# Performance work log

Measured on AMD Instinct MI355X. Metric: run time of the kernel, lower is better.

The kernel has to match this reference:

```python
import jax, jax.numpy as jnp
import numpy as np

INPUT_DIM, HIDDEN_DIM, OUTPUT_DIM, NUM_LAYERS = 128, 512, 128, 2
B, T = 32, 2048


def setup_inputs() -> dict:
    key = jax.random.key(0)
    ks = jax.random.split(key, 11)
    s_in = 1.0 / np.sqrt(HIDDEN_DIM)
    inp = {"x": jax.random.normal(ks[0], (B, T, INPUT_DIM), dtype=jnp.float32)}
    # layer 0 (input_dim -> hidden), layer 1 (hidden -> hidden); PyTorch gate order i,f,g,o
    inp["w_ih0"] = jax.random.uniform(ks[1], (4 * HIDDEN_DIM, INPUT_DIM), minval=-s_in, maxval=s_in)
    inp["w_hh0"] = jax.random.uniform(ks[2], (4 * HIDDEN_DIM, HIDDEN_DIM), minval=-s_in, maxval=s_in)
    inp["b_ih0"] = jax.random.uniform(ks[3], (4 * HIDDEN_DIM,), minval=-s_in, maxval=s_in)
    inp["b_hh0"] = jax.random.uniform(ks[4], (4 * HIDDEN_DIM,), minval=-s_in, maxval=s_in)
    inp["w_ih1"] = jax.random.uniform(ks[5], (4 * HIDDEN_DIM, HIDDEN_DIM), minval=-s_in, maxval=s_in)
    inp["w_hh1"] = jax.random.uniform(ks[6], (4 * HIDDEN_DIM, HIDDEN_DIM), minval=-s_in, maxval=s_in)
    inp["b_ih1"] = jax.random.uniform(ks[7], (4 * HIDDEN_DIM,), minval=-s_in, maxval=s_in)
    inp["b_hh1"] = jax.random.uniform(ks[8], (4 * HIDDEN_DIM,), minval=-s_in, maxval=s_in)
    inp["fc_w"] = jax.random.uniform(ks[9], (OUTPUT_DIM, HIDDEN_DIM), minval=-s_in, maxval=s_in)
    inp["fc_b"] = jax.random.uniform(ks[10], (OUTPUT_DIM,), minval=-s_in, maxval=s_in)
    return inp


def _lstm_layer(x, w_ih, w_hh, b_ih, b_hh):
    # x: [B, T, D] -> hidden states [B, T, H], final (h, c) each [B, H]
    b, t, _ = x.shape
    h4 = w_hh.shape[0]
    H = h4 // 4
    # precompute input projections for all timesteps (one big GEMM)
    x_proj = jnp.einsum('btd,gd->btg', x, w_ih) + b_ih + b_hh  # [B, T, 4H]

    def step(carry, xt):
        h, c = carry
        gates = xt + h @ w_hh.T  # [B, 4H]
        i, f, g, o = jnp.split(gates, 4, axis=-1)
        i = jax.nn.sigmoid(i)
        f = jax.nn.sigmoid(f)
        g = jnp.tanh(g)
        o = jax.nn.sigmoid(o)
        c = f * c + i * g
        h = o * jnp.tanh(c)
        return (h, c), h

    init = (jnp.zeros((b, H), x.dtype), jnp.zeros((b, H), x.dtype))
    (h_n, c_n), hs = jax.lax.scan(step, init, jnp.swapaxes(x_proj, 0, 1))
    return jnp.swapaxes(hs, 0, 1), h_n, c_n


def reference(x, w_ih0, w_hh0, b_ih0, b_hh0, w_ih1, w_hh1, b_ih1, b_hh1, fc_w, fc_b):
    out0, h0, c0 = _lstm_layer(x, w_ih0, w_hh0, b_ih0, b_hh0)
    out1, h1, c1 = _lstm_layer(out0, w_ih1, w_hh1, b_ih1, b_hh1)
    h_n = jnp.stack([h0, h1])  # [L, B, H]
    c_n = jnp.stack([c0, c1])  # [L, B, H]
    # fc(relu(.)) applied once over all (batch, time) -- collapses the Python loop
    output = jnp.einsum('bth,oh->bto', jax.nn.relu(out1), fc_w) + fc_b  # [B, T, O]
    hidden = jnp.einsum('lbh,oh->lbo', jax.nn.relu(h_n), fc_w) + fc_b   # [L, B, O]
    return jnp.squeeze(output), hidden, c_n
```

## Files before the change

kernel.cpp:

```cpp
#include <hip/hip_runtime.h>

typedef unsigned int u32;
typedef unsigned short u16;
typedef unsigned long long u64;

#define T_STEPS 2048
#define BATCH   32
#define HID     512
#define INDIM   128
#define OUTD    128
#define NG      2048
#define L0_WGS  64
#define L1_WGS  64
#define FC_WGS  4
#define NWG     (L0_WGS + L1_WGS + FC_WGS)
#define BH      (BATCH * HID)

#define HID_OFF 8388608
#define CN_OFF  8396800

#define WS_FLAGS   0
#define WS_H0RING  16384
#define WS_H1RING  (WS_H0RING + 131072)
#define WS_BIAS0   (WS_H1RING + 131072)
#define WS_BIAS1   (WS_BIAS0 + 8192)
#define WS_WFC     (WS_BIAS1 + 8192)
#define WS_WL0     (WS_WFC + 131072)
#define WS_WL1     (WS_WL0 + 2621440)
#define WS_XBF     (WS_WL1 + 4194304)

typedef __bf16 bf16x8 __attribute__((ext_vector_type(8)));
typedef float  f32x4  __attribute__((ext_vector_type(4)));
typedef unsigned int u32x4 __attribute__((ext_vector_type(4)));

__device__ __forceinline__ u16 f2bf(float f) {
    u32 u = __float_as_uint(f);
    u32 r = u + 0x7FFFu + ((u >> 16) & 1u);
    return (u16)(r >> 16);
}

union UB2 { u32x4 u; bf16x8 b; };
__device__ __forceinline__ bf16x8 as_bf(u32x4 u) { UB2 x; x.u = u; return x.b; }

__device__ __forceinline__ u32 relu2(u32 u) {
    u32 lo = (u & 0x8000u)     ? 0u : (u & 0xFFFFu);
    u32 hi = (u & 0x80000000u) ? 0u : (u & 0xFFFF0000u);
    return lo | hi;
}

__device__ __forceinline__ u32x4 ld16_llc(const void* p) {
    u32x4 r;
    asm volatile("global_load_dwordx4 %0, %1, off sc0 sc1"
                 : "=v"(r) : "v"(p) : "memory");
    return r;
}
__device__ __forceinline__ void wait_vm0() {
    asm volatile("s_waitcnt vmcnt(0)" ::: "memory");
    __builtin_amdgcn_sched_barrier(0);
}
__device__ __forceinline__ void vm0() {
    asm volatile("s_waitcnt vmcnt(0)" ::: "memory");
}


__global__ void k_zero(u32* dst, int n) {
    int i = blockIdx.x * blockDim.x + threadIdx.x;
    if (i < n) dst[i] = 0u;
}

__global__ void k_bias(const float* __restrict__ bih0, const float* __restrict__ bhh0,
                       const float* __restrict__ bih1, const float* __restrict__ bhh1,
                       float* __restrict__ bias0, float* __restrict__ bias1) {
    int i = blockIdx.x * blockDim.x + threadIdx.x;
    if (i < NG) {
        int orig = (i & 3) * HID + (i >> 2);
        bias0[i] = bih0[orig] + bhh0[orig];
        bias1[i] = bih1[orig] + bhh1[orig];
    }
}

__global__ void k_xconv(const float* __restrict__ x, u16* __restrict__ xbf) {
    int i = blockIdx.x * blockDim.x + threadIdx.x;
    float4 v = reinterpret_cast<const float4*>(x)[i];
    u32 lo = (u32)f2bf(v.x) | ((u32)f2bf(v.y) << 16);
    u32 hi = (u32)f2bf(v.z) | ((u32)f2bf(v.w) << 16);
    reinterpret_cast<uint2*>(xbf)[i] = make_uint2(lo, hi);
}

__global__ void k_wconv(const float* __restrict__ wih0, const float* __restrict__ whh0,
                        const float* __restrict__ wih1, const float* __restrict__ whh1,
                        const float* __restrict__ fcw,
                        u16* __restrict__ wl0, u16* __restrict__ wl1, u16* __restrict__ wfc) {
    int i = blockIdx.x * blockDim.x + threadIdx.x;
    if (i < 64 * 20480) {
        int wg = i / 20480, r = i % 20480;
        int ks = r / 1024, kb = (r % 1024) / 256, n = (r % 256) / 8, j = r % 8;
        int k = ks * 32 + kb * 8 + j;
        int p = wg * 32 + n;
        int orig = (p & 3) * HID + (p >> 2);
        float v = (k < HID) ? whh0[orig * HID + k] : wih0[orig * INDIM + (k - HID)];
        wl0[i] = f2bf(v);
        return;
    }
    int i1 = i - 64 * 20480;
    if (i1 < 64 * 32768) {
        int wg = i1 / 32768, r = i1 % 32768;
        int ks = r / 1024, kb = (r % 1024) / 256, n = (r % 256) / 8, j = r % 8;
        int k = ks * 32 + kb * 8 + j;
        int p = wg * 32 + n;
        int orig = (p & 3) * HID + (p >> 2);
        float v = (k < HID) ? wih1[orig * HID + k] : whh1[orig * HID + (k - HID)];
        wl1[i1] = f2bf(v);
        return;
    }
    int i2 = i1 - 64 * 32768;
    if (i2 < 4 * 16384) {
        int wg = i2 / 16384, r = i2 % 16384;
        int ks = r / 1024, kb = (r % 1024) / 256, n = (r % 256) / 8, j = r % 8;
        int k = ks * 32 + kb * 8 + j;
        int o = wg * 32 + n;
        wfc[i2] = f2bf(fcw[o * HID + k]);
    }
}


__global__ __launch_bounds__(256, 1)
void k_lstm(const u16* __restrict__ xbf,
            const u16* __restrict__ wl0g, const u16* __restrict__ wl1g, const u16* __restrict__ wfcg,
            const float* __restrict__ bias0, const float* __restrict__ bias1, const float* __restrict__ fcb,
            u16* __restrict__ h0ring, u16* __restrict__ h1ring,
            u32* __restrict__ flags, float* __restrict__ dout)
{
    __shared__ u16   wlds[32768];
    __shared__ u32x4 hstage[2][2048];
    const int tid  = threadIdx.x;
    const int lane = tid & 63;
    const int wv   = tid >> 6;
    const int mt   = wv >> 1;
    const int nt   = wv & 1;
    const int ci   = lane & 15;
    const int quad = lane >> 4;
    const int wg   = blockIdx.x;

    int role, rwg;
    if      (wg < L0_WGS)           { role = 0; rwg = wg; }
    else if (wg < L0_WGS + L1_WGS)  { role = 1; rwg = wg - L0_WGS; }
    else                            { role = 2; rwg = wg - L0_WGS - L1_WGS; }

    u32* flagL0 = flags;
    u32* flagL1 = flags + 64 * 16;
    u32* flagFC = flags + 128 * 16;
    u32* myflag = flags + wg * 16;

    {
        const u16* src = (role == 0) ? (wl0g + rwg * 20480)
                       : (role == 1) ? (wl1g + rwg * 32768)
                                     : (wfcg + rwg * 16384);
        const int n4 = (role == 0) ? 2560 : (role == 1) ? 4096 : 2048;
        uint4* d4 = reinterpret_cast<uint4*>(wlds);
        const uint4* s4 = reinterpret_cast<const uint4*>(src);
        for (int i = tid; i < n4; i += 256) d4[i] = s4[i];
    }
    __syncthreads();

    const bf16x8* wp = reinterpret_cast<const bf16x8*>(wlds);
    const int wbase  = quad * 32 + nt * 16 + ci;
    const int pcol   = rwg * 32 + nt * 16 + ci;
    const int gateid = pcol & 3;
    const float bias = (role == 0) ? bias0[pcol] : (role == 1) ? bias1[pcol] : fcb[pcol];
    const int brow0  = mt * 16 + quad * 4;
    const int arow   = mt * 16 + ci;
    const int jidx   = pcol >> 2;
    const int hfrag  = arow * 64 + quad;
    const int hswz   = arow & 7;

    float cst[4] = {0.f, 0.f, 0.f, 0.f};

    auto spin = [&](u32* f, int target) {
        if (target > 0)
            while ((int)__hip_atomic_load(f, __ATOMIC_RELAXED, __HIP_MEMORY_SCOPE_AGENT) < target)
                __builtin_amdgcn_s_sleep(1);
    };

    auto stage1 = [&](const u16* slot, int buf) {
        u32x4 b[8];
        #pragma unroll
        for (int r = 0; r < 8; ++r) b[r] = ld16_llc(slot + (tid + r * 256) * 8);
        wait_vm0();
        #pragma unroll
        for (int r = 0; r < 8; ++r) {
            int c = tid + r * 256;
            hstage[buf][c ^ ((c >> 6) & 7)] = b[r];
        }
    };
    auto stage2 = [&](const u16* s0, const u16* s1) {
        u32x4 b0[8], b1[8];
        #pragma unroll
        for (int r = 0; r < 8; ++r) b0[r] = ld16_llc(s0 + (tid + r * 256) * 8);
        #pragma unroll
        for (int r = 0; r < 8; ++r) b1[r] = ld16_llc(s1 + (tid + r * 256) * 8);
        wait_vm0();
        #pragma unroll
        for (int r = 0; r < 8; ++r) {
            int c = tid + r * 256;
            int cs = c ^ ((c >> 6) & 7);
            hstage[0][cs] = b0[r];
            hstage[1][cs] = b1[r];
        }
    };

    auto epi = [&](const f32x4& acc, u16* slotb) {
        float ga[4], hv[4];
        #pragma unroll
        for (int r = 0; r < 4; ++r) {
            float g  = acc[r] + bias;
            float sv = 1.0f / (1.0f + __expf(-g));
            float tv = 1.0f - 2.0f / (__expf(2.0f * g) + 1.0f);
            ga[r] = (gateid == 2) ? tv : sv;
        }
        const int bl = lane & ~3;
        #pragma unroll
        for (int r = 0; r < 4; ++r) {
            float iv = __shfl(ga[r], bl + 0);
            float fv = __shfl(ga[r], bl + 1);
            float gv = __shfl(ga[r], bl + 2);
            float ov = __shfl(ga[r], bl + 3);
            float cn = fv * cst[r] + iv * gv;
            cst[r] = cn;
            hv[r] = ov * (1.0f - 2.0f / (__expf(2.0f * cn) + 1.0f));
        }
        u32 lo = 0, hi = 0;
        #pragma unroll
        for (int r = 0; r < 4; ++r) {
            float c0 = __shfl(hv[r], (quad << 4) + 0);
            float c1 = __shfl(hv[r], (quad << 4) + 4);
            float c2 = __shfl(hv[r], (quad << 4) + 8);
            float c3 = __shfl(hv[r], (quad << 4) + 12);
            if (ci == r) {
                lo = (u32)f2bf(c0) | ((u32)f2bf(c1) << 16);
                hi = (u32)f2bf(c2) | ((u32)f2bf(c3) << 16);
            }
        }
        if (ci < 4) {
            u64* dst = reinterpret_cast<u64*>(slotb) + (brow0 + ci) * 128 + rwg * 2 + nt;
            u64 val = (u64)lo | ((u64)hi << 32);
            __hip_atomic_store(dst, val, __ATOMIC_RELAXED, __HIP_MEMORY_SCOPE_AGENT);
        }
    };

    #define HMFMA16S(BUF, KSOFF)                                                 \
        _Pragma("unroll")                                                        \
        for (int _k = 0; _k < 16; ++_k) {                                        \
          u32x4 _hv = hstage[BUF][(hfrag + _k * 4) ^ hswz];                      \
          bf16x8 _bv = wp[wbase + (_k + (KSOFF)) * 128];                         \
          if (_k & 1) accB = __builtin_amdgcn_mfma_f32_16x16x32_bf16(as_bf(_hv), _bv, accB, 0, 0, 0); \
          else        accA = __builtin_amdgcn_mfma_f32_16x16x32_bf16(as_bf(_hv), _bv, accA, 0, 0, 0); \
        }

    auto fcTileS = [&](int buf) -> f32x4 {
        f32x4 accA = {0.f,0.f,0.f,0.f}, accB = {0.f,0.f,0.f,0.f};
        #pragma unroll
        for (int ks = 0; ks < 16; ++ks) {
            u32x4 v = hstage[buf][(hfrag + ks * 4) ^ hswz];
            v[0] = relu2(v[0]); v[1] = relu2(v[1]); v[2] = relu2(v[2]); v[3] = relu2(v[3]);
            bf16x8 bv = wp[wbase + ks * 128];
            if (ks & 1) accB = __builtin_amdgcn_mfma_f32_16x16x32_bf16(as_bf(v), bv, accB, 0, 0, 0);
            else        accA = __builtin_amdgcn_mfma_f32_16x16x32_bf16(as_bf(v), bv, accA, 0, 0, 0);
        }
        return accA + accB;
    };

    if (role == 0) {
        u32* pf = (tid < 64) ? (flagL0 + tid * 16) : (tid < 128) ? (flagL1 + (tid - 64) * 16) : nullptr;
        const int po = (tid < 64) ? 0 : -3;
        for (int t = 0; t < T_STEPS; ++t) {
            const u16* xA = xbf + (arow * T_STEPS + t) * INDIM + quad * 8;
            f32x4 accA = {0.f, 0.f, 0.f, 0.f}, accB = {0.f, 0.f, 0.f, 0.f};
            u32x4 xv[4];
            #pragma unroll
            for (int k4 = 0; k4 < 4; ++k4) xv[k4] = *reinterpret_cast<const u32x4*>(xA + k4 * 32);
            #pragma unroll
            for (int k4 = 0; k4 < 4; ++k4) {
                bf16x8 bv = wp[wbase + (16 + k4) * 128];
                if (k4 & 1) accB = __builtin_amdgcn_mfma_f32_16x16x32_bf16(as_bf(xv[k4]), bv, accB, 0, 0, 0);
                else        accA = __builtin_amdgcn_mfma_f32_16x16x32_bf16(as_bf(xv[k4]), bv, accA, 0, 0, 0);
            }
            if (pf) spin(pf, t + po);
            __syncthreads();
            stage1(h0ring + ((t + 3) & 3) * BH, 0);
            __syncthreads();
            HMFMA16S(0, 0);
            epi(accA + accB, h0ring + (t & 3) * BH);
            vm0();
            __syncthreads();
            if (tid == 0)
                __hip_atomic_store(myflag, (u32)(t + 1), __ATOMIC_RELAXED, __HIP_MEMORY_SCOPE_AGENT);
        }
    } else if (role == 1) {
        u32* pf = (tid < 64)  ? (flagL0 + tid * 16)
                : (tid < 128) ? (flagL1 + (tid - 64) * 16)
                : (tid < 132) ? (flagFC + (tid - 128) * 16) : nullptr;
        const int po = (tid < 64) ? 1 : (tid < 128) ? 0 : -3;
        for (int t = 0; t < T_STEPS; ++t) {
            if (pf) spin(pf, t + po);
            __syncthreads();
            stage2(h0ring + (t & 3) * BH,
                   h1ring + ((t + 3) & 3) * BH);
            __syncthreads();
            f32x4 accA = {0.f, 0.f, 0.f, 0.f}, accB = {0.f, 0.f, 0.f, 0.f};
            HMFMA16S(0, 0);
            HMFMA16S(1, 16);
            epi(accA + accB, h1ring + (t & 3) * BH);
            vm0();
            __syncthreads();
            if (tid == 0)
                __hip_atomic_store(myflag, (u32)(t + 1), __ATOMIC_RELAXED, __HIP_MEMORY_SCOPE_AGENT);
        }
    } else {
        u32* pf = (tid < 64) ? (flagL1 + tid * 16) : nullptr;
        for (int t = 0; t < T_STEPS; ++t) {
            if (pf) spin(pf, t + 1);
            __syncthreads();
            stage1(h1ring + (t & 3) * BH, 0);
            __syncthreads();
            f32x4 acc = fcTileS(0);
            #pragma unroll
            for (int r = 0; r < 4; ++r)
                dout[((brow0 + r) * T_STEPS + t) * OUTD + pcol] = acc[r] + bias;
            __syncthreads();
            if (tid == 0)
                __hip_atomic_store(myflag, (u32)(t + 1), __ATOMIC_RELAXED, __HIP_MEMORY_SCOPE_AGENT);
        }
        stage1(h0ring + 3 * BH, 1);
        __syncthreads();
        f32x4 hh1 = fcTileS(0);
        f32x4 hh0 = fcTileS(1);
        #pragma unroll
        for (int r = 0; r < 4; ++r)
            dout[HID_OFF + (brow0 + r) * OUTD + pcol] = hh0[r] + bias;
        #pragma unroll
        for (int r = 0; r < 4; ++r)
            dout[HID_OFF + (BATCH + brow0 + r) * OUTD + pcol] = hh1[r] + bias;
    }

    if (role <= 1 && (ci & 3) == 0) {
        #pragma unroll
        for (int r = 0; r < 4; ++r)
            dout[CN_OFF + (role * BATCH + brow0 + r) * HID + jidx] = cst[r];
    }
}


extern "C" void kernel_launch(void* const* d_in, const int* in_sizes, int n_in,
                              void* d_out, int out_size, void* d_ws, size_t ws_size,
                              hipStream_t stream) {
    const float* x    = (const float*)d_in[0];
    const float* wih0 = (const float*)d_in[1];
    const float* whh0 = (const float*)d_in[2];
    const float* bih0 = (const float*)d_in[3];
    const float* bhh0 = (const float*)d_in[4];
    const float* wih1 = (const float*)d_in[5];
    const float* whh1 = (const float*)d_in[6];
    const float* bih1 = (const float*)d_in[7];
    const float* bhh1 = (const float*)d_in[8];
    const float* fcw  = (const float*)d_in[9];
    const float* fcb  = (const float*)d_in[10];

    char* ws = (char*)d_ws;
    u32*  flags = (u32*)(ws + WS_FLAGS);
    u16*  h0r   = (u16*)(ws + WS_H0RING);
    u16*  h1r   = (u16*)(ws + WS_H1RING);
    float* b0   = (float*)(ws + WS_BIAS0);
    float* b1   = (float*)(ws + WS_BIAS1);
    u16*  wfc   = (u16*)(ws + WS_WFC);
    u16*  wl0   = (u16*)(ws + WS_WL0);
    u16*  wl1   = (u16*)(ws + WS_WL1);
    u16*  xbf   = (u16*)(ws + WS_XBF);
    float* dout = (float*)d_out;

    k_zero<<<272, 256, 0, stream>>>((u32*)ws, 69632);
    k_bias<<<8, 256, 0, stream>>>(bih0, bhh0, bih1, bhh1, b0, b1);
    k_xconv<<<8192, 256, 0, stream>>>(x, xbf);
    k_wconv<<<13568, 256, 0, stream>>>(wih0, whh0, wih1, whh1, fcw, wl0, wl1, wfc);
    k_lstm<<<NWG, 256, 0, stream>>>(xbf, wl0, wl1, wfc, b0, b1, fcb,
                                    h0r, h1r, flags, dout);
}
```

Measured before the change: 8.986 ms.

## Use full-length hidden-state history buffers to drop ring backpressure waits

When the workspace is large enough, each layer writes its hidden states to a distinct slot per timestep instead of a 4-deep ring. This removes the backpressure spins where producers waited on consumers (layer 0 on layer 1, layer 1 on the FC workgroups), so the three pipeline stages can drift apart freely. Because no slot is ever rewritten, loads switch from LLC-coherent sc0 sc1 to sc0 only. The cost is about 128 MB of extra workspace, and the new path only runs if the harness supplies that much.

After: 9.059 ms. About the same (+0.8%).

```diff
diff --git a/kernel.cpp b/kernel.cpp
--- a/kernel.cpp
+++ b/kernel.cpp
@@ -28,6 +28,9 @@
 #define WS_WL0     (WS_WFC + 131072)
 #define WS_WL1     (WS_WL0 + 2621440)
 #define WS_XBF     (WS_WL1 + 4194304)
+#define WS_H0DEEP  (WS_XBF + 16777216)
+#define WS_H1DEEP  (WS_H0DEEP + 67141632)
+#define WS_DEEPEND (WS_H1DEEP + 67141632)
 
 typedef __bf16 bf16x8 __attribute__((ext_vector_type(8)));
 typedef float  f32x4  __attribute__((ext_vector_type(4)));
@@ -51,6 +54,12 @@
 __device__ __forceinline__ u32x4 ld16_llc(const void* p) {
     u32x4 r;
     asm volatile("global_load_dwordx4 %0, %1, off sc0 sc1"
+                 : "=v"(r) : "v"(p) : "memory");
+    return r;
+}
+__device__ __forceinline__ u32x4 ld16_l2(const void* p) {
+    u32x4 r;
+    asm volatile("global_load_dwordx4 %0, %1, off sc0"
                  : "=v"(r) : "v"(p) : "memory");
     return r;
 }
@@ -129,7 +138,7 @@
             const u16* __restrict__ wl0g, const u16* __restrict__ wl1g, const u16* __restrict__ wfcg,
             const float* __restrict__ bias0, const float* __restrict__ bias1, const float* __restrict__ fcb,
             u16* __restrict__ h0ring, u16* __restrict__ h1ring,
-            u32* __restrict__ flags, float* __restrict__ dout)
+            u32* __restrict__ flags, float* __restrict__ dout, const int deep)
 {
     __shared__ u16   wlds[32768];
     __shared__ u32x4 hstage[2][2048];
@@ -182,10 +191,19 @@
                 __builtin_amdgcn_s_sleep(1);
     };
 
+    auto rdIdx = [&](int t_h) -> long {
+        return deep ? (long)(t_h + 1) : (long)(t_h & 3);
+    };
+
     auto stage1 = [&](const u16* slot, int buf) {
         u32x4 b[8];
-        #pragma unroll
-        for (int r = 0; r < 8; ++r) b[r] = ld16_llc(slot + (tid + r * 256) * 8);
+        if (deep) {
+            #pragma unroll
+            for (int r = 0; r < 8; ++r) b[r] = ld16_l2(slot + (tid + r * 256) * 8);
+        } else {
+            #pragma unroll
+            for (int r = 0; r < 8; ++r) b[r] = ld16_llc(slot + (tid + r * 256) * 8);
+        }
         wait_vm0();
         #pragma unroll
         for (int r = 0; r < 8; ++r) {
@@ -195,10 +213,17 @@
     };
     auto stage2 = [&](const u16* s0, const u16* s1) {
         u32x4 b0[8], b1[8];
-        #pragma unroll
-        for (int r = 0; r < 8; ++r) b0[r] = ld16_llc(s0 + (tid + r * 256) * 8);
-        #pragma unroll
-        for (int r = 0; r < 8; ++r) b1[r] = ld16_llc(s1 + (tid + r * 256) * 8);
+        if (deep) {
+            #pragma unroll
+            for (int r = 0; r < 8; ++r) b0[r] = ld16_l2(s0 + (tid + r * 256) * 8);
+            #pragma unroll
+            for (int r = 0; r < 8; ++r) b1[r] = ld16_l2(s1 + (tid + r * 256) * 8);
+        } else {
+            #pragma unroll
+            for (int r = 0; r < 8; ++r) b0[r] = ld16_llc(s0 + (tid + r * 256) * 8);
+            #pragma unroll
+            for (int r = 0; r < 8; ++r) b1[r] = ld16_llc(s1 + (tid + r * 256) * 8);
+        }
         wait_vm0();
         #pragma unroll
         for (int r = 0; r < 8; ++r) {
@@ -271,7 +296,8 @@
     };
 
     if (role == 0) {
-        u32* pf = (tid < 64) ? (flagL0 + tid * 16) : (tid < 128) ? (flagL1 + (tid - 64) * 16) : nullptr;
+        u32* pf = (tid < 64) ? (flagL0 + tid * 16)
+                : (!deep && tid < 128) ? (flagL1 + (tid - 64) * 16) : nullptr;
         const int po = (tid < 64) ? 0 : -3;
         for (int t = 0; t < T_STEPS; ++t) {
             const u16* xA = xbf + (arow * T_STEPS + t) * INDIM + quad * 8;
@@ -287,10 +313,10 @@
             }
             if (pf) spin(pf, t + po);
             __syncthreads();
-            stage1(h0ring + ((t + 3) & 3) * BH, 0);
+            stage1(h0ring + rdIdx(t - 1) * BH, 0);
             __syncthreads();
             HMFMA16S(0, 0);
-            epi(accA + accB, h0ring + (t & 3) * BH);
+            epi(accA + accB, h0ring + rdIdx(t) * BH);
             vm0();
             __syncthreads();
             if (tid == 0)
@@ -299,18 +325,18 @@
     } else if (role == 1) {
         u32* pf = (tid < 64)  ? (flagL0 + tid * 16)
                 : (tid < 128) ? (flagL1 + (tid - 64) * 16)
-                : (tid < 132) ? (flagFC + (tid - 128) * 16) : nullptr;
+                : (!deep && tid < 132) ? (flagFC + (tid - 128) * 16) : nullptr;
         const int po = (tid < 64) ? 1 : (tid < 128) ? 0 : -3;
         for (int t = 0; t < T_STEPS; ++t) {
             if (pf) spin(pf, t + po);
             __syncthreads();
-            stage2(h0ring + (t & 3) * BH,
-                   h1ring + ((t + 3) & 3) * BH);
+            stage2(h0ring + rdIdx(t) * BH,
+                   h1ring + rdIdx(t - 1) * BH);
             __syncthreads();
             f32x4 accA = {0.f, 0.f, 0.f, 0.f}, accB = {0.f, 0.f, 0.f, 0.f};
             HMFMA16S(0, 0);
             HMFMA16S(1, 16);
-            epi(accA + accB, h1ring + (t & 3) * BH);
+            epi(accA + accB, h1ring + rdIdx(t) * BH);
             vm0();
             __syncthreads();
             if (tid == 0)
@@ -321,7 +347,7 @@
         for (int t = 0; t < T_STEPS; ++t) {
             if (pf) spin(pf, t + 1);
             __syncthreads();
-            stage1(h1ring + (t & 3) * BH, 0);
+            stage1(h1ring + rdIdx(t) * BH, 0);
             __syncthreads();
             f32x4 acc = fcTileS(0);
             #pragma unroll
@@ -331,7 +357,7 @@
             if (tid == 0)
                 __hip_atomic_store(myflag, (u32)(t + 1), __ATOMIC_RELAXED, __HIP_MEMORY_SCOPE_AGENT);
         }
-        stage1(h0ring + 3 * BH, 1);
+        stage1(h0ring + rdIdx(T_STEPS - 1) * BH, 1);
         __syncthreads();
         f32x4 hh1 = fcTileS(0);
         f32x4 hh0 = fcTileS(1);
@@ -368,8 +394,6 @@
 
     char* ws = (char*)d_ws;
     u32*  flags = (u32*)(ws + WS_FLAGS);
-    u16*  h0r   = (u16*)(ws + WS_H0RING);
-    u16*  h1r   = (u16*)(ws + WS_H1RING);
     float* b0   = (float*)(ws + WS_BIAS0);
     float* b1   = (float*)(ws + WS_BIAS1);
     u16*  wfc   = (u16*)(ws + WS_WFC);
@@ -378,10 +402,20 @@
     u16*  xbf   = (u16*)(ws + WS_XBF);
     float* dout = (float*)d_out;
 
-    k_zero<<<272, 256, 0, stream>>>((u32*)ws, 69632);
+    const int deep = (ws_size >= (size_t)WS_DEEPEND) ? 1 : 0;
+    u16* h0r = deep ? (u16*)(ws + WS_H0DEEP) : (u16*)(ws + WS_H0RING);
+    u16* h1r = deep ? (u16*)(ws + WS_H1DEEP) : (u16*)(ws + WS_H1RING);
+
+    if (deep) {
+        k_zero<<<16, 256, 0, stream>>>((u32*)ws, 4096);
+        k_zero<<<32, 256, 0, stream>>>((u32*)(ws + WS_H0DEEP), 8192);
+        k_zero<<<32, 256, 0, stream>>>((u32*)(ws + WS_H1DEEP), 8192);
+    } else {
+        k_zero<<<272, 256, 0, stream>>>((u32*)ws, 69632);
+    }
     k_bias<<<8, 256, 0, stream>>>(bih0, bhh0, bih1, bhh1, b0, b1);
     k_xconv<<<8192, 256, 0, stream>>>(x, xbf);
     k_wconv<<<13568, 256, 0, stream>>>(wih0, whh0, wih1, whh1, fcw, wl0, wl1, wfc);
     k_lstm<<<NWG, 256, 0, stream>>>(xbf, wl0, wl1, wfc, b0, b1, fcb,
-                                    h0r, h1r, flags, dout);
-}
+                                    h0r, h1r, flags, dout, deep);
+}
```

## Halve persistent workgroup count with 512-thread blocks and stream layer-1 weights

Applied to the files above, without the earlier changes.

Restructures the persistent LSTM kernel to use half as many workgroups (32+32+2) with 512 threads each, so every block owns 64 gate columns. Fewer participants in each step's flag barrier should shorten the per-step cross-workgroup sync. Layer 1 now keeps only half its weights in LDS and reads the recurrent half from global memory. It also splits its staging so the MFMAs on the first h buffer run while the second load is still in flight. Layer 0 moves the input-projection MFMAs for the next step off the critical path, after the epilogue. The cost is more work per block per step and extra global weight traffic for layer 1.

New measurement: 10.58 ms. +17.7%, slower.

```diff
diff --git a/kernel.cpp b/kernel.cpp
--- a/kernel.cpp
+++ b/kernel.cpp
@@ -10,10 +10,11 @@
 #define INDIM   128
 #define OUTD    128
 #define NG      2048
-#define L0_WGS  64
-#define L1_WGS  64
-#define FC_WGS  4
+#define L0_WGS  32
+#define L1_WGS  32
+#define FC_WGS  2
 #define NWG     (L0_WGS + L1_WGS + FC_WGS)
+#define NTHR    512
 #define BH      (BATCH * HID)
 
 #define HID_OFF 8388608
@@ -58,6 +59,10 @@
     asm volatile("s_waitcnt vmcnt(0)" ::: "memory");
     __builtin_amdgcn_sched_barrier(0);
 }
+__device__ __forceinline__ void wait_vm4() {
+    asm volatile("s_waitcnt vmcnt(4)" ::: "memory");
+    __builtin_amdgcn_sched_barrier(0);
+}
 __device__ __forceinline__ void vm0() {
     asm volatile("s_waitcnt vmcnt(0)" ::: "memory");
 }
@@ -92,52 +97,52 @@
                         const float* __restrict__ fcw,
                         u16* __restrict__ wl0, u16* __restrict__ wl1, u16* __restrict__ wfc) {
     int i = blockIdx.x * blockDim.x + threadIdx.x;
-    if (i < 64 * 20480) {
-        int wg = i / 20480, r = i % 20480;
-        int ks = r / 1024, kb = (r % 1024) / 256, n = (r % 256) / 8, j = r % 8;
+    if (i < 32 * 40960) {
+        int wg = i / 40960, r = i % 40960;
+        int ks = r / 2048, kb = (r % 2048) / 512, n = (r % 512) / 8, j = r % 8;
         int k = ks * 32 + kb * 8 + j;
-        int p = wg * 32 + n;
+        int p = wg * 64 + n;
         int orig = (p & 3) * HID + (p >> 2);
         float v = (k < HID) ? whh0[orig * HID + k] : wih0[orig * INDIM + (k - HID)];
         wl0[i] = f2bf(v);
         return;
     }
-    int i1 = i - 64 * 20480;
-    if (i1 < 64 * 32768) {
-        int wg = i1 / 32768, r = i1 % 32768;
-        int ks = r / 1024, kb = (r % 1024) / 256, n = (r % 256) / 8, j = r % 8;
+    int i1 = i - 32 * 40960;
+    if (i1 < 32 * 65536) {
+        int wg = i1 / 65536, r = i1 % 65536;
+        int ks = r / 2048, kb = (r % 2048) / 512, n = (r % 512) / 8, j = r % 8;
         int k = ks * 32 + kb * 8 + j;
-        int p = wg * 32 + n;
+        int p = wg * 64 + n;
         int orig = (p & 3) * HID + (p >> 2);
         float v = (k < HID) ? wih1[orig * HID + k] : whh1[orig * HID + (k - HID)];
         wl1[i1] = f2bf(v);
         return;
     }
-    int i2 = i1 - 64 * 32768;
-    if (i2 < 4 * 16384) {
-        int wg = i2 / 16384, r = i2 % 16384;
-        int ks = r / 1024, kb = (r % 1024) / 256, n = (r % 256) / 8, j = r % 8;
+    int i2 = i1 - 32 * 65536;
+    if (i2 < 2 * 32768) {
+        int wg = i2 / 32768, r = i2 % 32768;
+        int ks = r / 2048, kb = (r % 2048) / 512, n = (r % 512) / 8, j = r % 8;
         int k = ks * 32 + kb * 8 + j;
-        int o = wg * 32 + n;
+        int o = wg * 64 + n;
         wfc[i2] = f2bf(fcw[o * HID + k]);
     }
 }
 
 
-__global__ __launch_bounds__(256, 1)
+__global__ __launch_bounds__(NTHR, 1)
 void k_lstm(const u16* __restrict__ xbf,
             const u16* __restrict__ wl0g, const u16* __restrict__ wl1g, const u16* __restrict__ wfcg,
             const float* __restrict__ bias0, const float* __restrict__ bias1, const float* __restrict__ fcb,
             u16* __restrict__ h0ring, u16* __restrict__ h1ring,
             u32* __restrict__ flags, float* __restrict__ dout)
 {
-    __shared__ u16   wlds[32768];
-    __shared__ u32x4 hstage[2][2048];
+    __shared__ u16   wlds[40960];
+    __shared__ u32x4 hstage[2048];
     const int tid  = threadIdx.x;
     const int lane = tid & 63;
     const int wv   = tid >> 6;
-    const int mt   = wv >> 1;
-    const int nt   = wv & 1;
+    const int mt   = wv >> 2;
+    const int nc   = wv & 3;
     const int ci   = lane & 15;
     const int quad = lane >> 4;
     const int wg   = blockIdx.x;
@@ -150,22 +155,23 @@
     u32* flagL0 = flags;
     u32* flagL1 = flags + 64 * 16;
     u32* flagFC = flags + 128 * 16;
-    u32* myflag = flags + wg * 16;
+    u32* myflag = (role == 0) ? (flagL0 + rwg * 16)
+                : (role == 1) ? (flagL1 + rwg * 16) : (flagFC + rwg * 16);
 
     {
-        const u16* src = (role == 0) ? (wl0g + rwg * 20480)
-                       : (role == 1) ? (wl1g + rwg * 32768)
-                                     : (wfcg + rwg * 16384);
-        const int n4 = (role == 0) ? 2560 : (role == 1) ? 4096 : 2048;
+        const u16* src = (role == 0) ? (wl0g + rwg * 40960)
+                       : (role == 1) ? (wl1g + rwg * 65536)
+                                     : (wfcg + rwg * 32768);
+        const int n4 = (role == 0) ? 5120 : 4096;
         uint4* d4 = reinterpret_cast<uint4*>(wlds);
         const uint4* s4 = reinterpret_cast<const uint4*>(src);
-        for (int i = tid; i < n4; i += 256) d4[i] = s4[i];
+        for (int i = tid; i < n4; i += NTHR) d4[i] = s4[i];
     }
     __syncthreads();
 
     const bf16x8* wp = reinterpret_cast<const bf16x8*>(wlds);
-    const int wbase  = quad * 32 + nt * 16 + ci;
-    const int pcol   = rwg * 32 + nt * 16 + ci;
+    const int wbase  = quad * 64 + nc * 16 + ci;
+    const int pcol   = rwg * 64 + nc * 16 + ci;
     const int gateid = pcol & 3;
     const float bias = (role == 0) ? bias0[pcol] : (role == 1) ? bias1[pcol] : fcb[pcol];
     const int brow0  = mt * 16 + quad * 4;
@@ -181,32 +187,19 @@
             while ((int)__hip_atomic_load(f, __ATOMIC_RELAXED, __HIP_MEMORY_SCOPE_AGENT) < target)
                 __builtin_amdgcn_s_sleep(1);
     };
-
-    auto stage1 = [&](const u16* slot, int buf) {
-        u32x4 b[8];
-        #pragma unroll
-        for (int r = 0; r < 8; ++r) b[r] = ld16_llc(slot + (tid + r * 256) * 8);
+    auto stf = [&](u32* f, u32 v) {
+        __hip_atomic_store(f, v, __ATOMIC_RELAXED, __HIP_MEMORY_SCOPE_AGENT);
+    };
+
+    auto scat = [&](int c, u32x4 b) { hstage[c ^ ((c >> 6) & 7)] = b; };
+
+    auto stage1 = [&](const u16* slot) {
+        u32x4 b[4];
+        #pragma unroll
+        for (int r = 0; r < 4; ++r) b[r] = ld16_llc(slot + (tid + r * 512) * 8);
         wait_vm0();
         #pragma unroll
-        for (int r = 0; r < 8; ++r) {
-            int c = tid + r * 256;
-            hstage[buf][c ^ ((c >> 6) & 7)] = b[r];
-        }
-    };
-    auto stage2 = [&](const u16* s0, const u16* s1) {
-        u32x4 b0[8], b1[8];
-        #pragma unroll
-        for (int r = 0; r < 8; ++r) b0[r] = ld16_llc(s0 + (tid + r * 256) * 8);
-        #pragma unroll
-        for (int r = 0; r < 8; ++r) b1[r] = ld16_llc(s1 + (tid + r * 256) * 8);
-        wait_vm0();
-        #pragma unroll
-        for (int r = 0; r < 8; ++r) {
-            int c = tid + r * 256;
-            int cs = c ^ ((c >> 6) & 7);
-            hstage[0][cs] = b0[r];
-            hstage[1][cs] = b1[r];
-        }
+        for (int r = 0; r < 4; ++r) scat(tid + r * 512, b[r]);
     };
 
     auto epi = [&](const f32x4& acc, u16* slotb) {
@@ -242,28 +235,28 @@
             }
         }
         if (ci < 4) {
-            u64* dst = reinterpret_cast<u64*>(slotb) + (brow0 + ci) * 128 + rwg * 2 + nt;
+            u64* dst = reinterpret_cast<u64*>(slotb) + (brow0 + ci) * 128 + rwg * 4 + nc;
             u64 val = (u64)lo | ((u64)hi << 32);
             __hip_atomic_store(dst, val, __ATOMIC_RELAXED, __HIP_MEMORY_SCOPE_AGENT);
         }
     };
 
-    #define HMFMA16S(BUF, KSOFF)                                                 \
+    #define HMFMA16L(KSOFF)                                                      \
         _Pragma("unroll")                                                        \
         for (int _k = 0; _k < 16; ++_k) {                                        \
-          u32x4 _hv = hstage[BUF][(hfrag + _k * 4) ^ hswz];                      \
-          bf16x8 _bv = wp[wbase + (_k + (KSOFF)) * 128];                         \
+          u32x4 _hv = hstage[(hfrag + _k * 4) ^ hswz];                           \
+          bf16x8 _bv = wp[wbase + (_k + (KSOFF)) * 256];                         \
           if (_k & 1) accB = __builtin_amdgcn_mfma_f32_16x16x32_bf16(as_bf(_hv), _bv, accB, 0, 0, 0); \
           else        accA = __builtin_amdgcn_mfma_f32_16x16x32_bf16(as_bf(_hv), _bv, accA, 0, 0, 0); \
         }
 
-    auto fcTileS = [&](int buf) -> f32x4 {
+    auto fcTileS = [&]() -> f32x4 {
         f32x4 accA = {0.f,0.f,0.f,0.f}, accB = {0.f,0.f,0.f,0.f};
         #pragma unroll
         for (int ks = 0; ks < 16; ++ks) {
-            u32x4 v = hstage[buf][(hfrag + ks * 4) ^ hswz];
+            u32x4 v = hstage[(hfrag + ks * 4) ^ hswz];
             v[0] = relu2(v[0]); v[1] = relu2(v[1]); v[2] = relu2(v[2]); v[3] = relu2(v[3]);
-            bf16x8 bv = wp[wbase + ks * 128];
+            bf16x8 bv = wp[wbase + ks * 256];
             if (ks & 1) accB = __builtin_amdgcn_mfma_f32_16x16x32_bf16(as_bf(v), bv, accB, 0, 0, 0);
             else        accA = __builtin_amdgcn_mfma_f32_16x16x32_bf16(as_bf(v), bv, accA, 0, 0, 0);
         }
@@ -271,70 +264,97 @@
     };
 
     if (role == 0) {
-        u32* pf = (tid < 64) ? (flagL0 + tid * 16) : (tid < 128) ? (flagL1 + (tid - 64) * 16) : nullptr;
-        const int po = (tid < 64) ? 0 : -3;
-        for (int t = 0; t < T_STEPS; ++t) {
+        u32* pf = (tid < 32) ? (flagL0 + tid * 16)
+                : (tid >= 64 && tid < 96) ? (flagL1 + (tid - 64) * 16) : nullptr;
+        const int po = (tid < 32) ? 0 : -3;
+        auto xpart = [&](int t, f32x4& aA, f32x4& aB) {
             const u16* xA = xbf + (arow * T_STEPS + t) * INDIM + quad * 8;
-            f32x4 accA = {0.f, 0.f, 0.f, 0.f}, accB = {0.f, 0.f, 0.f, 0.f};
             u32x4 xv[4];
             #pragma unroll
             for (int k4 = 0; k4 < 4; ++k4) xv[k4] = *reinterpret_cast<const u32x4*>(xA + k4 * 32);
             #pragma unroll
             for (int k4 = 0; k4 < 4; ++k4) {
-                bf16x8 bv = wp[wbase + (16 + k4) * 128];
-                if (k4 & 1) accB = __builtin_amdgcn_mfma_f32_16x16x32_bf16(as_bf(xv[k4]), bv, accB, 0, 0, 0);
-                else        accA = __builtin_amdgcn_mfma_f32_16x16x32_bf16(as_bf(xv[k4]), bv, accA, 0, 0, 0);
+                bf16x8 bv = wp[wbase + (16 + k4) * 256];
+                if (k4 & 1) aB = __builtin_amdgcn_mfma_f32_16x16x32_bf16(as_bf(xv[k4]), bv, aB, 0, 0, 0);
+                else        aA = __builtin_amdgcn_mfma_f32_16x16x32_bf16(as_bf(xv[k4]), bv, aA, 0, 0, 0);
             }
-            if (pf) spin(pf, t + po);
-            __syncthreads();
-            stage1(h0ring + ((t + 3) & 3) * BH, 0);
-            __syncthreads();
-            HMFMA16S(0, 0);
-            epi(accA + accB, h0ring + (t & 3) * BH);
-            vm0();
-            __syncthreads();
-            if (tid == 0)
-                __hip_atomic_store(myflag, (u32)(t + 1), __ATOMIC_RELAXED, __HIP_MEMORY_SCOPE_AGENT);
-        }
-    } else if (role == 1) {
-        u32* pf = (tid < 64)  ? (flagL0 + tid * 16)
-                : (tid < 128) ? (flagL1 + (tid - 64) * 16)
-                : (tid < 132) ? (flagFC + (tid - 128) * 16) : nullptr;
-        const int po = (tid < 64) ? 1 : (tid < 128) ? 0 : -3;
+        };
+        f32x4 xA0 = {0.f,0.f,0.f,0.f}, xB0 = {0.f,0.f,0.f,0.f};
+        xpart(0, xA0, xB0);
         for (int t = 0; t < T_STEPS; ++t) {
             if (pf) spin(pf, t + po);
             __syncthreads();
-            stage2(h0ring + (t & 3) * BH,
-                   h1ring + ((t + 3) & 3) * BH);
-            __syncthreads();
-            f32x4 accA = {0.f, 0.f, 0.f, 0.f}, accB = {0.f, 0.f, 0.f, 0.f};
-            HMFMA16S(0, 0);
-            HMFMA16S(1, 16);
+            stage1(h0ring + ((t + 3) & 3) * BH);
+            __syncthreads();
+            f32x4 accA = xA0, accB = xB0;
+            HMFMA16L(0);
+            epi(accA + accB, h0ring + (t & 3) * BH);
+            if (t + 1 < T_STEPS) {
+                xA0 = (f32x4){0.f,0.f,0.f,0.f}; xB0 = (f32x4){0.f,0.f,0.f,0.f};
+                xpart(t + 1, xA0, xB0);
+            }
+            vm0();
+            __syncthreads();
+            if (tid == 0) stf(myflag, (u32)(t + 1));
+        }
+    } else if (role == 1) {
+        u32* pf = (tid < 32)  ? (flagL0 + tid * 16)
+                : (tid >= 64 && tid < 96) ? (flagL1 + (tid - 64) * 16)
+                : (tid >= 128 && tid < 130) ? (flagFC + (tid - 128) * 16) : nullptr;
+        const int po = (tid < 32) ? 1 : (tid < 96) ? 0 : -3;
+        const u16* wB = wl1g + rwg * 65536 + 32768 + quad * 512 + (nc * 16 + ci) * 8;
+        for (int t = 0; t < T_STEPS; ++t) {
+            if (pf) spin(pf, t + po);
+            __syncthreads();
+            const u16* s0 = h0ring + (t & 3) * BH;
+            const u16* s1 = h1ring + ((t + 3) & 3) * BH;
+            u32x4 b0[4], b1[4];
+            #pragma unroll
+            for (int r = 0; r < 4; ++r) b0[r] = ld16_llc(s0 + (tid + r * 512) * 8);
+            #pragma unroll
+            for (int r = 0; r < 4; ++r) b1[r] = ld16_llc(s1 + (tid + r * 512) * 8);
+            wait_vm4();
+            #pragma unroll
+            for (int r = 0; r < 4; ++r) scat(tid + r * 512, b0[r]);
+            __syncthreads();
+            f32x4 accA = {0.f,0.f,0.f,0.f}, accB = {0.f,0.f,0.f,0.f};
+            HMFMA16L(0);
+            __syncthreads();
+            wait_vm0();
+            #pragma unroll
+            for (int r = 0; r < 4; ++r) scat(tid + r * 512, b1[r]);
+            __syncthreads();
+            #pragma unroll
+            for (int _k = 0; _k < 16; ++_k) {
+                u32x4 hv = hstage[(hfrag + _k * 4) ^ hswz];
+                bf16x8 bv = *reinterpret_cast<const bf16x8*>(wB + _k * 2048);
+                if (_k & 1) accB = __builtin_amdgcn_mfma_f32_16x16x32_bf16(as_bf(hv), bv, accB, 0, 0, 0);
+                else        accA = __builtin_amdgcn_mfma_f32_16x16x32_bf16(as_bf(hv), bv, accA, 0, 0, 0);
+            }
             epi(accA + accB, h1ring + (t & 3) * BH);
             vm0();
             __syncthreads();
-            if (tid == 0)
-                __hip_atomic_store(myflag, (u32)(t + 1), __ATOMIC_RELAXED, __HIP_MEMORY_SCOPE_AGENT);
+            if (tid == 0) stf(myflag, (u32)(t + 1));
         }
     } else {
-        u32* pf = (tid < 64) ? (flagL1 + tid * 16) : nullptr;
+        u32* pf = (tid < 32) ? (flagL1 + tid * 16) : nullptr;
         for (int t = 0; t < T_STEPS; ++t) {
             if (pf) spin(pf, t + 1);
             __syncthreads();
-            stage1(h1ring + (t & 3) * BH, 0);
-            __syncthreads();
-            f32x4 acc = fcTileS(0);
+            stage1(h1ring + (t & 3) * BH);
+            __syncthreads();
+            f32x4 acc = fcTileS();
             #pragma unroll
             for (int r = 0; r < 4; ++r)
                 dout[((brow0 + r) * T_STEPS + t) * OUTD + pcol] = acc[r] + bias;
             __syncthreads();
-            if (tid == 0)
-                __hip_atomic_store(myflag, (u32)(t + 1), __ATOMIC_RELAXED, __HIP_MEMORY_SCOPE_AGENT);
-        }
-        stage1(h0ring + 3 * BH, 1);
+            if (tid == 0) stf(myflag, (u32)(t + 1));
+        }
+        f32x4 hh1 = fcTileS();
         __syncthreads();
-        f32x4 hh1 = fcTileS(0);
-        f32x4 hh0 = fcTileS(1);
+        stage1(h0ring + 3 * BH);
+        __syncthreads();
+        f32x4 hh0 = fcTileS();
         #pragma unroll
         for (int r = 0; r < 4; ++r)
             dout[HID_OFF + (brow0 + r) * OUTD + pcol] = hh0[r] + bias;
@@ -382,6 +402,6 @@
     k_bias<<<8, 256, 0, stream>>>(bih0, bhh0, bih1, bhh1, b0, b1);
     k_xconv<<<8192, 256, 0, stream>>>(x, xbf);
     k_wconv<<<13568, 256, 0, stream>>>(wih0, whh0, wih1, whh1, fcw, wl0, wl1, wfc);
-    k_lstm<<<NWG, 256, 0, stream>>>(xbf, wl0, wl1, wfc, b0, b1, fcb,
-                                    h0r, h1r, flags, dout);
-}
+    k_lstm<<<NWG, NTHR, 0, stream>>>(xbf, wl0, wl1, wfc, b0, b1, fcb,
+                                     h0r, h1r, flags, dout);
+}
```

## Per-wave flag spinning, overlap x-projection and ring loads with dependency waits

Applied to the files above, without the earlier changes.

Each wave now polls the producer flags itself (lane-indexed) rather than a subset of threads spinning and then a block barrier, which removes one __syncthreads per step. Layer 0 computes the next step's input projection after the epilogue, taking it off the critical path. Both LSTM roles also issue their global ring loads before waiting on the slack/back-pressure flags. This shortens the serial per-timestep recurrence latency, at the cost of more flag polling traffic and subtler memory-ordering assumptions.

After: 9.252 ms. 3.0% more time.

```diff
diff --git a/kernel.cpp b/kernel.cpp
--- a/kernel.cpp
+++ b/kernel.cpp
@@ -181,32 +181,24 @@
             while ((int)__hip_atomic_load(f, __ATOMIC_RELAXED, __HIP_MEMORY_SCOPE_AGENT) < target)
                 __builtin_amdgcn_s_sleep(1);
     };
-
-    auto stage1 = [&](const u16* slot, int buf) {
-        u32x4 b[8];
-        #pragma unroll
-        for (int r = 0; r < 8; ++r) b[r] = ld16_llc(slot + (tid + r * 256) * 8);
-        wait_vm0();
+    auto stf = [&](u32* f, u32 v) {
+        __hip_atomic_store(f, v, __ATOMIC_RELAXED, __HIP_MEMORY_SCOPE_AGENT);
+    };
+
+    auto scat = [&](int buf, u32x4* b) {
         #pragma unroll
         for (int r = 0; r < 8; ++r) {
             int c = tid + r * 256;
             hstage[buf][c ^ ((c >> 6) & 7)] = b[r];
         }
     };
-    auto stage2 = [&](const u16* s0, const u16* s1) {
-        u32x4 b0[8], b1[8];
-        #pragma unroll
-        for (int r = 0; r < 8; ++r) b0[r] = ld16_llc(s0 + (tid + r * 256) * 8);
-        #pragma unroll
-        for (int r = 0; r < 8; ++r) b1[r] = ld16_llc(s1 + (tid + r * 256) * 8);
+
+    auto stage1 = [&](const u16* slot, int buf) {
+        u32x4 b[8];
+        #pragma unroll
+        for (int r = 0; r < 8; ++r) b[r] = ld16_llc(slot + (tid + r * 256) * 8);
         wait_vm0();
-        #pragma unroll
-        for (int r = 0; r < 8; ++r) {
-            int c = tid + r * 256;
-            int cs = c ^ ((c >> 6) & 7);
-            hstage[0][cs] = b0[r];
-            hstage[1][cs] = b1[r];
-        }
+        scat(buf, b);
     };
 
     auto epi = [&](const f32x4& acc, u16* slotb) {
@@ -271,41 +263,59 @@
     };
 
     if (role == 0) {
-        u32* pf = (tid < 64) ? (flagL0 + tid * 16) : (tid < 128) ? (flagL1 + (tid - 64) * 16) : nullptr;
-        const int po = (tid < 64) ? 0 : -3;
-        for (int t = 0; t < T_STEPS; ++t) {
+        f32x4 xA0 = {0.f,0.f,0.f,0.f}, xB0 = {0.f,0.f,0.f,0.f};
+        auto xpart = [&](int t) {
             const u16* xA = xbf + (arow * T_STEPS + t) * INDIM + quad * 8;
-            f32x4 accA = {0.f, 0.f, 0.f, 0.f}, accB = {0.f, 0.f, 0.f, 0.f};
             u32x4 xv[4];
             #pragma unroll
             for (int k4 = 0; k4 < 4; ++k4) xv[k4] = *reinterpret_cast<const u32x4*>(xA + k4 * 32);
             #pragma unroll
             for (int k4 = 0; k4 < 4; ++k4) {
                 bf16x8 bv = wp[wbase + (16 + k4) * 128];
-                if (k4 & 1) accB = __builtin_amdgcn_mfma_f32_16x16x32_bf16(as_bf(xv[k4]), bv, accB, 0, 0, 0);
-                else        accA = __builtin_amdgcn_mfma_f32_16x16x32_bf16(as_bf(xv[k4]), bv, accA, 0, 0, 0);
+                if (k4 & 1) xB0 = __builtin_amdgcn_mfma_f32_16x16x32_bf16(as_bf(xv[k4]), bv, xB0, 0, 0, 0);
+                else        xA0 = __builtin_amdgcn_mfma_f32_16x16x32_bf16(as_bf(xv[k4]), bv, xA0, 0, 0, 0);
             }
-            if (pf) spin(pf, t + po);
-            __syncthreads();
-            stage1(h0ring + ((t + 3) & 3) * BH, 0);
-            __syncthreads();
+        };
+        xpart(0);
+        for (int t = 0; t < T_STEPS; ++t) {
+            spin(flagL0 + lane * 16, t);
+            u32x4 b[8];
+            const u16* hA = h0ring + ((t + 3) & 3) * BH;
+            #pragma unroll
+            for (int r = 0; r < 8; ++r) b[r] = ld16_llc(hA + (tid + r * 256) * 8);
+            if (tid >= 64 && tid < 128)
+                spin(flagL1 + (tid - 64) * 16, t - 3);
+            wait_vm0();
+            scat(0, b);
+            __syncthreads();
+            f32x4 accA = xA0, accB = xB0;
             HMFMA16S(0, 0);
             epi(accA + accB, h0ring + (t & 3) * BH);
+            if (t + 1 < T_STEPS) {
+                xA0 = (f32x4){0.f,0.f,0.f,0.f}; xB0 = (f32x4){0.f,0.f,0.f,0.f};
+                xpart(t + 1);
+            }
             vm0();
             __syncthreads();
-            if (tid == 0)
-                __hip_atomic_store(myflag, (u32)(t + 1), __ATOMIC_RELAXED, __HIP_MEMORY_SCOPE_AGENT);
+            if (tid == 0) stf(myflag, (u32)(t + 1));
         }
     } else if (role == 1) {
-        u32* pf = (tid < 64)  ? (flagL0 + tid * 16)
-                : (tid < 128) ? (flagL1 + (tid - 64) * 16)
-                : (tid < 132) ? (flagFC + (tid - 128) * 16) : nullptr;
-        const int po = (tid < 64) ? 1 : (tid < 128) ? 0 : -3;
         for (int t = 0; t < T_STEPS; ++t) {
-            if (pf) spin(pf, t + po);
-            __syncthreads();
-            stage2(h0ring + (t & 3) * BH,
-                   h1ring + ((t + 3) & 3) * BH);
+            spin(flagL1 + lane * 16, t);
+            u32x4 b1[8];
+            const u16* s1 = h1ring + ((t + 3) & 3) * BH;
+            #pragma unroll
+            for (int r = 0; r < 8; ++r) b1[r] = ld16_llc(s1 + (tid + r * 256) * 8);
+            if (tid >= 128 && tid < 132)
+                spin(flagFC + (tid - 128) * 16, t - 3);
+            spin(flagL0 + lane * 16, t + 1);
+            u32x4 b0[8];
+            const u16* s0 = h0ring + (t & 3) * BH;
+            #pragma unroll
+            for (int r = 0; r < 8; ++r) b0[r] = ld16_llc(s0 + (tid + r * 256) * 8);
+            wait_vm0();
+            scat(0, b0);
+            scat(1, b1);
             __syncthreads();
             f32x4 accA = {0.f, 0.f, 0.f, 0.f}, accB = {0.f, 0.f, 0.f, 0.f};
             HMFMA16S(0, 0);
@@ -313,13 +323,11 @@
             epi(accA + accB, h1ring + (t & 3) * BH);
             vm0();
             __syncthreads();
-            if (tid == 0)
-                __hip_atomic_store(myflag, (u32)(t + 1), __ATOMIC_RELAXED, __HIP_MEMORY_SCOPE_AGENT);
+            if (tid == 0) stf(myflag, (u32)(t + 1));
         }
     } else {
-        u32* pf = (tid < 64) ? (flagL1 + tid * 16) : nullptr;
         for (int t = 0; t < T_STEPS; ++t) {
-            if (pf) spin(pf, t + 1);
+            spin(flagL1 + lane * 16, t + 1);
             __syncthreads();
             stage1(h1ring + (t & 3) * BH, 0);
             __syncthreads();
@@ -328,8 +336,7 @@
             for (int r = 0; r < 4; ++r)
                 dout[((brow0 + r) * T_STEPS + t) * OUTD + pcol] = acc[r] + bias;
             __syncthreads();
-            if (tid == 0)
-                __hip_atomic_store(myflag, (u32)(t + 1), __ATOMIC_RELAXED, __HIP_MEMORY_SCOPE_AGENT);
+            if (tid == 0) stf(myflag, (u32)(t + 1));
         }
         stage1(h0ring + 3 * BH, 1);
         __syncthreads();
```
